# Performance work log

Hardware: AMD Instinct MI355X
Metric: run time of the kernel (lower is better)

The kernel has to match this reference:

```python
import jax, jax.numpy as jnp
import numpy as np

B, N, D_IN, D_OUT, H = 2, 2048, 1024, 1024, 16
HEAD_DIM = D_OUT // H


def setup_inputs() -> dict:
    key = jax.random.key(0)
    ks = jax.random.split(key, 8)
    s = 0.02
    return {
        "x": jax.random.normal(ks[0], (B, N, D_IN), dtype=jnp.float32),
        "Wq": jax.random.normal(ks[1], (D_IN, D_OUT), dtype=jnp.float32) * s,
        "Wk": jax.random.normal(ks[2], (D_IN, D_OUT), dtype=jnp.float32) * s,
        "Wv": jax.random.normal(ks[3], (D_IN, D_OUT), dtype=jnp.float32) * s,
        "Wo": jax.random.normal(ks[4], (D_OUT, D_OUT), dtype=jnp.float32) * s,
        "bo": jnp.zeros((D_OUT,), dtype=jnp.float32),
        "w": jax.random.uniform(ks[5], (H,), dtype=jnp.float32),
        "v": jax.random.uniform(ks[6], (H,), dtype=jnp.float32),
    }


def reference(x, Wq, Wk, Wv, Wo, bo, w, v):
    b, n, _ = x.shape
    h = w.shape[0]
    hd = Wq.shape[1] // h

    # QKV projections -> [b, h, n, hd]
    def proj(W):
        return (x @ W).reshape(b, n, h, hd).transpose(0, 2, 1, 3)

    q, k, val = proj(Wq), proj(Wk), proj(Wv)

    # relative-distance decay R_hat: [h, n, n]
    pos = jnp.arange(n)
    R = jnp.abs(pos[:, None] - pos[None, :]).astype(x.dtype)  # [n, n]
    wv = w[:, None, None]
    vv = v[:, None, None]
    R_hat = (1.0 + jnp.exp(vv)) / (1.0 + jnp.exp(vv - wv * R))  # [h, n, n]

    # ReLU(QK^T) * R_hat, causal mask, scaled softmax
    scores = jax.nn.relu(jnp.einsum("bhqd,bhkd->bhqk", q, k)) * R_hat[None]
    causal = jnp.triu(jnp.ones((n, n), dtype=bool), k=1)
    scores = jnp.where(causal[None, None], -jnp.inf, scores)
    attn = jax.nn.softmax(scores / np.sqrt(hd).astype(x.dtype), axis=-1)

    ctx = jnp.einsum("bhqk,bhkd->bhqd", attn, val)
    ctx = ctx.transpose(0, 2, 1, 3).reshape(b, n, h * hd)
    return ctx @ Wo + bo
```

## Files before the change

kernel.cpp:

```cpp
#include <hip/hip_runtime.h>

typedef unsigned short u16;
typedef unsigned int u32;
typedef __attribute__((ext_vector_type(8))) short bf16x8;
typedef __attribute__((ext_vector_type(4))) float f32x4;

__device__ __forceinline__ u16 f2bf(float f) {
    u32 u = __float_as_uint(f);
    u += 0x7fffu + ((u >> 16) & 1u);
    return (u16)(u >> 16);
}

#define GL2LDS(gp, lp)                                                                 \
    __builtin_amdgcn_global_load_lds((const __attribute__((address_space(1))) u32*)(const void*)(gp), \
                                     (__attribute__((address_space(3))) u32*)(void*)(lp), 16, 0, 0)

__global__ __launch_bounds__(256) void cast_kernel(const float* __restrict__ src,
                                                   u16* __restrict__ dst, int n4) {
    int i = blockIdx.x * 256 + threadIdx.x;
    if (i >= n4) return;
    float4 val = ((const float4*)src)[i];
    uint2 o;
    o.x = ((u32)f2bf(val.y) << 16) | f2bf(val.x);
    o.y = ((u32)f2bf(val.w) << 16) | f2bf(val.z);
    ((uint2*)dst)[i] = o;
}

__global__ __launch_bounds__(256) void transpose4(const float* __restrict__ Wq,
                                                  const float* __restrict__ Wk,
                                                  const float* __restrict__ Wv,
                                                  const float* __restrict__ Wo,
                                                  u16* __restrict__ Wcat,
                                                  u16* __restrict__ Wot) {
    __shared__ float tl[32][33];
    const int zi = blockIdx.z;
    const float* src = (zi == 0) ? Wq : (zi == 1) ? Wk : (zi == 2) ? Wv : Wo;
    u16* dst = (zi < 3) ? (Wcat + zi * 1048576) : Wot;
    const int tx = threadIdx.x & 31, ty = threadIdx.x >> 5;
    const int kt = blockIdx.y * 32, nt = blockIdx.x * 32;
#pragma unroll
    for (int j = 0; j < 4; ++j)
        tl[ty + j * 8][tx] = src[(kt + ty + j * 8) * 1024 + nt + tx];
    __syncthreads();
#pragma unroll
    for (int j = 0; j < 4; ++j)
        dst[(nt + ty + j * 8) * 1024 + kt + tx] = f2bf(tl[tx][ty + j * 8]);
}

__global__ __launch_bounds__(256) void transpose_v(const u16* __restrict__ src,
                                                   u16* __restrict__ dst) {
    __shared__ u16 tl[64][68];
    const int t = threadIdx.x, tx = t & 15, ty = t >> 4;
    const int rt = blockIdx.y * 64, ct = blockIdx.x * 64;
#pragma unroll
    for (int j = 0; j < 4; ++j) {
        const int row = ty + j * 16;
        uint2 vv = *(const uint2*)(src + (size_t)(rt + row) * 1024 + ct + tx * 4);
        tl[row][tx * 4 + 0] = (u16)(vv.x & 0xffff);
        tl[row][tx * 4 + 1] = (u16)(vv.x >> 16);
        tl[row][tx * 4 + 2] = (u16)(vv.y & 0xffff);
        tl[row][tx * 4 + 3] = (u16)(vv.y >> 16);
    }
    __syncthreads();
#pragma unroll
    for (int j = 0; j < 4; ++j) {
        const int c = ty + j * 16;
        uint2 o;
        o.x = (u32)tl[tx * 4 + 0][c] | ((u32)tl[tx * 4 + 1][c] << 16);
        o.y = (u32)tl[tx * 4 + 2][c] | ((u32)tl[tx * 4 + 3][c] << 16);
        *(uint2*)(dst + (size_t)(ct + c) * 4096 + rt + tx * 4) = o;
    }
}

__global__ __launch_bounds__(256) void rtab_kernel(const float* __restrict__ wp,
                                                   const float* __restrict__ vp,
                                                   float* __restrict__ tab,
                                                   u32* __restrict__ counter) {
    const int i = blockIdx.x * 256 + threadIdx.x;
    if (i == 0) counter[0] = 0u;
    const int h = i >> 11, d = i & 2047;
    const float vv = vp[h], ww = wp[h];
    tab[i] = (1.f + expf(vv)) / (1.f + expf(vv - ww * (float)d)) * 0.125f;
}

template <int MODE, int BN>
__global__ __launch_bounds__(256, 3) void gemm128(const u16* __restrict__ A,
                                                  const u16* __restrict__ Bt,
                                                  float* __restrict__ C,
                                                  const float* __restrict__ bias,
                                                  u16* __restrict__ Cb,
                                                  u16* __restrict__ Vrow,
                                                  int M, int N, int K) {
    constexpr int NBW = BN / 32;
    __shared__ __align__(16) u16 As[8192];
    __shared__ __align__(16) u16 Bs[BN * 64];
    const int t = threadIdx.x, lane = t & 63, wv = t >> 6;
    const int l15 = lane & 15, quad = lane >> 4;
    const int m0 = blockIdx.y << 7, n0 = blockIdx.x * BN;
    const int wm = (wv & 1) << 6, wn = (wv >> 1) * (BN / 2);

    f32x4 acc[4][NBW];
#pragma unroll
    for (int i = 0; i < 4; ++i)
#pragma unroll
        for (int j = 0; j < NBW; ++j) acc[i][j] = (f32x4){0.f, 0.f, 0.f, 0.f};

    const int lrow = lane >> 3, lchunk = lane & 7;
    for (int k0 = 0; k0 < K; k0 += 64) {
#pragma unroll
        for (int c = 0; c < 4; ++c) {
            const int r0 = wv * 32 + c * 8;
            const int row = r0 + lrow;
            const int g = lchunk ^ (row & 7);
            GL2LDS(A + (size_t)(m0 + row) * K + k0 + g * 8, &As[r0 * 64]);
        }
#pragma unroll
        for (int c = 0; c < BN / 32; ++c) {
            const int r0 = wv * (BN / 4) + c * 8;
            const int row = r0 + lrow;
            const int g = lchunk ^ (row & 7);
            GL2LDS(Bt + (size_t)(n0 + row) * K + k0 + g * 8, &Bs[r0 * 64]);
        }
        __syncthreads();
#pragma unroll
        for (int ks = 0; ks < 2; ++ks) {
            const int p = ((ks << 2) | quad) ^ (l15 & 7);
            bf16x8 af[4], bfr[NBW];
#pragma unroll
            for (int i = 0; i < 4; ++i)
                af[i] = *(const bf16x8*)&As[(wm + i * 16 + l15) * 64 + p * 8];
#pragma unroll
            for (int j = 0; j < NBW; ++j)
                bfr[j] = *(const bf16x8*)&Bs[(wn + j * 16 + l15) * 64 + p * 8];
#pragma unroll
            for (int mb = 0; mb < 4; ++mb)
#pragma unroll
                for (int nb = 0; nb < NBW; ++nb)
                    acc[mb][nb] = __builtin_amdgcn_mfma_f32_16x16x32_bf16(af[mb], bfr[nb],
                                                                          acc[mb][nb], 0, 0, 0);
        }
        __syncthreads();
    }
    const int rb = m0 + wm + (quad << 2);
    const int cbase = n0 + wn + l15;
#pragma unroll
    for (int mb = 0; mb < 4; ++mb)
#pragma unroll
        for (int nb = 0; nb < NBW; ++nb) {
            const int col = cbase + nb * 16;
#pragma unroll
            for (int r = 0; r < 4; ++r) {
                const int row = rb + mb * 16 + r;
                if (MODE == 0) {
                    C[(size_t)row * N + col] = acc[mb][nb][r] + bias[col];
                } else {
                    if (col < 2048)
                        Cb[(size_t)row * 2048 + col] = f2bf(acc[mb][nb][r]);
                    else
                        Vrow[(size_t)row * 1024 + (col - 2048)] = f2bf(acc[mb][nb][r]);
                }
            }
        }
}

__global__ __launch_bounds__(256, 3) void attn_kernel(const u16* __restrict__ qkb,
                                                      const u16* __restrict__ vtb,
                                                      const float* __restrict__ rtab,
                                                      u16* __restrict__ ctxb,
                                                      u32* __restrict__ counter) {
    __shared__ __align__(16) u16 Kt[2][4096];
    __shared__ __align__(16) u16 Vt2[2][4096];
    __shared__ float rall[2048];
    __shared__ int jobS;

    const int t = threadIdx.x, lane = t & 63, wv = t >> 6;
    const int l15 = lane & 15, quad = lane >> 4;
    const int lrow = lane >> 3, lchunk = lane & 7;
    const int half0 = (wv & 1) * 32;

    for (;;) {
        if (t == 0) jobS = (int)atomicAdd(counter, 1u);
        __syncthreads();
        const int job = jobS;
        if (job >= 1024) break;
        const int qt = 31 - (job >> 5);
        const int bh = job & 31;
        const int b = bh >> 4, h = bh & 15;
        const int q0 = qt << 6;

        for (int i = t; i < q0 + 64; i += 256) rall[i] = rtab[(h << 11) + i];

        bf16x8 qb[2];
        {
            const u16* qrow = qkb + (size_t)(b * 2048 + q0 + (wv << 4) + l15) * 2048 +
                              (h << 6) + quad * 8;
            qb[0] = *(const bf16x8*)(qrow);
            qb[1] = *(const bf16x8*)(qrow + 32);
        }

        f32x4 cacc[4];
#pragma unroll
        for (int i = 0; i < 4; ++i) cacc[i] = (f32x4){0.f, 0.f, 0.f, 0.f};
        float lacc = 0.f;

#pragma unroll
        for (int c = 0; c < 4; ++c) {
            const int r0 = half0 + c * 8;
            const int row = r0 + lrow;
            const int g = lchunk ^ (row & 7);
            if (wv < 2)
                GL2LDS(qkb + (size_t)(b * 2048 + row) * 2048 + 1024 + (h << 6) + g * 8,
                       &Kt[0][r0 * 64]);
            else
                GL2LDS(vtb + (size_t)((h << 6) + row) * 4096 + b * 2048 + g * 8,
                       &Vt2[0][r0 * 64]);
        }

        for (int kt = 0; kt <= qt; ++kt) {
            const int bsel = kt & 1;
            __syncthreads();
            if (kt < qt) {
                const int kg0 = (kt + 1) << 6;
#pragma unroll
                for (int c = 0; c < 4; ++c) {
                    const int r0 = half0 + c * 8;
                    const int row = r0 + lrow;
                    const int g = lchunk ^ (row & 7);
                    if (wv < 2)
                        GL2LDS(qkb + (size_t)(b * 2048 + kg0 + row) * 2048 + 1024 + (h << 6) + g * 8,
                               &Kt[bsel ^ 1][r0 * 64]);
                    else
                        GL2LDS(vtb + (size_t)((h << 6) + row) * 4096 + b * 2048 + kg0 + g * 8,
                               &Vt2[bsel ^ 1][r0 * 64]);
                }
            }

            f32x4 sacc[4];
#pragma unroll
            for (int i = 0; i < 4; ++i) sacc[i] = (f32x4){0.f, 0.f, 0.f, 0.f};
#pragma unroll
            for (int ks = 0; ks < 2; ++ks) {
                const int p = ((ks << 2) | quad) ^ (l15 & 7);
#pragma unroll
                for (int mb = 0; mb < 4; ++mb) {
                    bf16x8 ka = *(const bf16x8*)&Kt[bsel][(mb * 16 + l15) * 64 + p * 8];
                    sacc[mb] = __builtin_amdgcn_mfma_f32_16x16x32_bf16(ka, qb[ks],
                                                                       sacc[mb], 0, 0, 0);
                }
            }

            const int D0 = q0 - (kt << 6) + (wv << 4) + l15;
            u32 pk[4][2];
            if (kt < qt) {
#pragma unroll
                for (int mb = 0; mb < 4; ++mb) {
                    float pe[4];
#pragma unroll
                    for (int r = 0; r < 4; ++r) {
                        const int dist = D0 - (mb * 16 + (quad << 2) + r);
                        pe[r] = __expf(fmaxf(sacc[mb][r], 0.f) * rall[dist]);
                        lacc += pe[r];
                    }
                    pk[mb][0] = (__float_as_uint(pe[0]) >> 16) |
                                (__float_as_uint(pe[1]) & 0xffff0000u);
                    pk[mb][1] = (__float_as_uint(pe[2]) >> 16) |
                                (__float_as_uint(pe[3]) & 0xffff0000u);
                }
            } else {
#pragma unroll
                for (int mb = 0; mb < 4; ++mb) {
                    float pe[4];
#pragma unroll
                    for (int r = 0; r < 4; ++r) {
                        const int dist = D0 - (mb * 16 + (quad << 2) + r);
                        const int di = dist < 0 ? 0 : dist;
                        float p0 = __expf(fmaxf(sacc[mb][r], 0.f) * rall[di]);
                        pe[r] = (dist < 0) ? 0.f : p0;
                        lacc += pe[r];
                    }
                    pk[mb][0] = (__float_as_uint(pe[0]) >> 16) |
                                (__float_as_uint(pe[1]) & 0xffff0000u);
                    pk[mb][1] = (__float_as_uint(pe[2]) >> 16) |
                                (__float_as_uint(pe[3]) & 0xffff0000u);
                }
            }

#pragma unroll
            for (int ks = 0; ks < 2; ++ks) {
                int4 pv = {(int)pk[2 * ks][0], (int)pk[2 * ks][1],
                           (int)pk[2 * ks + 1][0], (int)pk[2 * ks + 1][1]};
                bf16x8 pb = *(bf16x8*)&pv;
                const int gA = (4 * ks + (quad >> 1)) ^ (l15 & 7);
                const int gB = (4 * ks + 2 + (quad >> 1)) ^ (l15 & 7);
                const int off = (quad & 1) * 4;
#pragma unroll
                for (int db = 0; db < 4; ++db) {
                    const u16* base = &Vt2[bsel][(db * 16 + l15) * 64];
                    uint2 va = *(const uint2*)(base + gA * 8 + off);
                    uint2 vb = *(const uint2*)(base + gB * 8 + off);
                    int4 vv = {(int)va.x, (int)va.y, (int)vb.x, (int)vb.y};
                    bf16x8 vf = *(bf16x8*)&vv;
                    cacc[db] = __builtin_amdgcn_mfma_f32_16x16x32_bf16(vf, pb,
                                                                       cacc[db], 0, 0, 0);
                }
            }
        }

        float lt = lacc;
        lt += __shfl_xor(lt, 16, 64);
        lt += __shfl_xor(lt, 32, 64);
        const float inv = 1.f / lt;
        u16* op = ctxb + (size_t)(b * 2048 + q0 + (wv << 4) + l15) * 1024 +
                  (h << 6) + (quad << 2);
#pragma unroll
        for (int db = 0; db < 4; ++db) {
            uint2 o;
            o.x = (u32)f2bf(cacc[db][0] * inv) | ((u32)f2bf(cacc[db][1] * inv) << 16);
            o.y = (u32)f2bf(cacc[db][2] * inv) | ((u32)f2bf(cacc[db][3] * inv) << 16);
            *(uint2*)(op + db * 16) = o;
        }
    }
}

extern "C" void kernel_launch(void* const* d_in, const int* in_sizes, int n_in,
                              void* d_out, int out_size, void* d_ws, size_t ws_size,
                              hipStream_t stream) {
    const float* x  = (const float*)d_in[0];
    const float* Wq = (const float*)d_in[1];
    const float* Wk = (const float*)d_in[2];
    const float* Wv = (const float*)d_in[3];
    const float* Wo = (const float*)d_in[4];
    const float* bo = (const float*)d_in[5];
    const float* w  = (const float*)d_in[6];
    const float* v  = (const float*)d_in[7];
    float* out = (float*)d_out;

    char* w8 = (char*)d_ws;
    u16*  xb   = (u16*)(w8);
    u16*  Wcat = (u16*)(w8 + (8u << 20));
    u16*  Wot  = (u16*)(w8 + (14u << 20));
    u16*  qkb  = (u16*)(w8 + (16u << 20));
    u16*  vtb  = (u16*)(w8 + (32u << 20));
    u16*  ctxb = (u16*)(w8 + (40u << 20));
    float* rtab = (float*)(w8 + (48u << 20));
    u32*  counter = (u32*)(w8 + (48u << 20) + (1u << 17));
    u16*  vrow = (u16*)(w8 + (49u << 20));

    cast_kernel<<<4096, 256, 0, stream>>>(x, xb, 1048576);
    transpose4<<<dim3(32, 32, 4), 256, 0, stream>>>(Wq, Wk, Wv, Wo, Wcat, Wot);
    rtab_kernel<<<128, 256, 0, stream>>>(w, v, rtab, counter);

    gemm128<1, 128><<<dim3(24, 32), 256, 0, stream>>>(xb, Wcat, nullptr, nullptr, qkb, vrow,
                                                      4096, 3072, 1024);
    transpose_v<<<dim3(16, 64), 256, 0, stream>>>(vrow, vtb);
    attn_kernel<<<768, 256, 0, stream>>>(qkb, vtb, rtab, ctxb, counter);
    gemm128<0, 64><<<dim3(16, 32), 256, 0, stream>>>(ctxb, Wot, out, bo, nullptr, nullptr,
                                                     4096, 1024, 1024);
}
```

Baseline: 193.3 us.

## Fuse V transpose into QKV GEMM epilogue, merge rtab into cast, single-buffer attention

The QKV GEMM now writes the V columns already transposed, staging the tile through swizzled LDS, so the separate transpose_v kernel and its round trip through memory go away. The rtab and counter init move into the cast kernel, removing another launch. The attention kernel drops K/V double buffering, which halves its LDS use, and raises occupancy to 6 blocks per CU with twice as many persistent blocks. The cost is that global loads no longer overlap the MFMA work and an extra barrier is added per tile.

```diff
diff --git a/kernel.cpp b/kernel.cpp
--- a/kernel.cpp
+++ b/kernel.cpp
@@ -16,8 +16,18 @@
                                      (__attribute__((address_space(3))) u32*)(void*)(lp), 16, 0, 0)
 
 __global__ __launch_bounds__(256) void cast_kernel(const float* __restrict__ src,
-                                                   u16* __restrict__ dst, int n4) {
+                                                   u16* __restrict__ dst, int n4,
+                                                   const float* __restrict__ wp,
+                                                   const float* __restrict__ vp,
+                                                   float* __restrict__ tab,
+                                                   u32* __restrict__ counter) {
     int i = blockIdx.x * 256 + threadIdx.x;
+    if (i == 0) counter[0] = 0u;
+    if (i < 32768) {
+        const int h = i >> 11, d = i & 2047;
+        const float vv = vp[h], ww = wp[h];
+        tab[i] = (1.f + expf(vv)) / (1.f + expf(vv - ww * (float)d)) * 0.125f;
+    }
     if (i >= n4) return;
     float4 val = ((const float4*)src)[i];
     uint2 o;
@@ -47,49 +57,13 @@
         dst[(nt + ty + j * 8) * 1024 + kt + tx] = f2bf(tl[tx][ty + j * 8]);
 }
 
-__global__ __launch_bounds__(256) void transpose_v(const u16* __restrict__ src,
-                                                   u16* __restrict__ dst) {
-    __shared__ u16 tl[64][68];
-    const int t = threadIdx.x, tx = t & 15, ty = t >> 4;
-    const int rt = blockIdx.y * 64, ct = blockIdx.x * 64;
-#pragma unroll
-    for (int j = 0; j < 4; ++j) {
-        const int row = ty + j * 16;
-        uint2 vv = *(const uint2*)(src + (size_t)(rt + row) * 1024 + ct + tx * 4);
-        tl[row][tx * 4 + 0] = (u16)(vv.x & 0xffff);
-        tl[row][tx * 4 + 1] = (u16)(vv.x >> 16);
-        tl[row][tx * 4 + 2] = (u16)(vv.y & 0xffff);
-        tl[row][tx * 4 + 3] = (u16)(vv.y >> 16);
-    }
-    __syncthreads();
-#pragma unroll
-    for (int j = 0; j < 4; ++j) {
-        const int c = ty + j * 16;
-        uint2 o;
-        o.x = (u32)tl[tx * 4 + 0][c] | ((u32)tl[tx * 4 + 1][c] << 16);
-        o.y = (u32)tl[tx * 4 + 2][c] | ((u32)tl[tx * 4 + 3][c] << 16);
-        *(uint2*)(dst + (size_t)(ct + c) * 4096 + rt + tx * 4) = o;
-    }
-}
-
-__global__ __launch_bounds__(256) void rtab_kernel(const float* __restrict__ wp,
-                                                   const float* __restrict__ vp,
-                                                   float* __restrict__ tab,
-                                                   u32* __restrict__ counter) {
-    const int i = blockIdx.x * 256 + threadIdx.x;
-    if (i == 0) counter[0] = 0u;
-    const int h = i >> 11, d = i & 2047;
-    const float vv = vp[h], ww = wp[h];
-    tab[i] = (1.f + expf(vv)) / (1.f + expf(vv - ww * (float)d)) * 0.125f;
-}
-
 template <int MODE, int BN>
 __global__ __launch_bounds__(256, 3) void gemm128(const u16* __restrict__ A,
                                                   const u16* __restrict__ Bt,
                                                   float* __restrict__ C,
                                                   const float* __restrict__ bias,
                                                   u16* __restrict__ Cb,
-                                                  u16* __restrict__ Vrow,
+                                                  u16* __restrict__ Vtb,
                                                   int M, int N, int K) {
     constexpr int NBW = BN / 32;
     __shared__ __align__(16) u16 As[8192];
@@ -141,6 +115,30 @@
         }
         __syncthreads();
     }
+    if (MODE == 1 && n0 >= 2048) {
+#pragma unroll
+        for (int mb = 0; mb < 4; ++mb)
+#pragma unroll
+            for (int nb = 0; nb < NBW; ++nb) {
+                const int c = wn + nb * 16 + l15;
+                u16* base = (c < 64 ? As : Bs) + (c & 63) * 128;
+#pragma unroll
+                for (int r = 0; r < 4; ++r) {
+                    const int rw = wm + mb * 16 + (quad << 2) + r;
+                    base[(((rw >> 3) ^ (c & 15)) << 3) + (rw & 7)] = f2bf(acc[mb][nb][r]);
+                }
+            }
+        __syncthreads();
+        const int c = t & 127, rseg = t >> 7;
+        const u16* base = (c < 64 ? As : Bs) + (c & 63) * 128;
+        u16* dst = Vtb + (size_t)(n0 - 2048 + c) * 4096 + m0 + rseg * 64;
+#pragma unroll
+        for (int ch = 0; ch < 8; ++ch) {
+            const int rc = rseg * 8 + ch;
+            *(uint4*)(dst + ch * 8) = *(const uint4*)&base[((rc ^ (c & 15)) << 3)];
+        }
+        return;
+    }
     const int rb = m0 + wm + (quad << 2);
     const int cbase = n0 + wn + l15;
 #pragma unroll
@@ -154,22 +152,19 @@
                 if (MODE == 0) {
                     C[(size_t)row * N + col] = acc[mb][nb][r] + bias[col];
                 } else {
-                    if (col < 2048)
-                        Cb[(size_t)row * 2048 + col] = f2bf(acc[mb][nb][r]);
-                    else
-                        Vrow[(size_t)row * 1024 + (col - 2048)] = f2bf(acc[mb][nb][r]);
-                }
-            }
-        }
-}
-
-__global__ __launch_bounds__(256, 3) void attn_kernel(const u16* __restrict__ qkb,
+                    Cb[(size_t)row * 2048 + col] = f2bf(acc[mb][nb][r]);
+                }
+            }
+        }
+}
+
+__global__ __launch_bounds__(256, 6) void attn_kernel(const u16* __restrict__ qkb,
                                                       const u16* __restrict__ vtb,
                                                       const float* __restrict__ rtab,
                                                       u16* __restrict__ ctxb,
                                                       u32* __restrict__ counter) {
-    __shared__ __align__(16) u16 Kt[2][4096];
-    __shared__ __align__(16) u16 Vt2[2][4096];
+    __shared__ __align__(16) u16 Kt[4096];
+    __shared__ __align__(16) u16 Vt[4096];
     __shared__ float rall[2048];
     __shared__ int jobS;
 
@@ -203,24 +198,10 @@
         for (int i = 0; i < 4; ++i) cacc[i] = (f32x4){0.f, 0.f, 0.f, 0.f};
         float lacc = 0.f;
 
-#pragma unroll
-        for (int c = 0; c < 4; ++c) {
-            const int r0 = half0 + c * 8;
-            const int row = r0 + lrow;
-            const int g = lchunk ^ (row & 7);
-            if (wv < 2)
-                GL2LDS(qkb + (size_t)(b * 2048 + row) * 2048 + 1024 + (h << 6) + g * 8,
-                       &Kt[0][r0 * 64]);
-            else
-                GL2LDS(vtb + (size_t)((h << 6) + row) * 4096 + b * 2048 + g * 8,
-                       &Vt2[0][r0 * 64]);
-        }
-
         for (int kt = 0; kt <= qt; ++kt) {
-            const int bsel = kt & 1;
+            const int kg0 = kt << 6;
             __syncthreads();
-            if (kt < qt) {
-                const int kg0 = (kt + 1) << 6;
+            {
 #pragma unroll
                 for (int c = 0; c < 4; ++c) {
                     const int r0 = half0 + c * 8;
@@ -228,12 +209,13 @@
                     const int g = lchunk ^ (row & 7);
                     if (wv < 2)
                         GL2LDS(qkb + (size_t)(b * 2048 + kg0 + row) * 2048 + 1024 + (h << 6) + g * 8,
-                               &Kt[bsel ^ 1][r0 * 64]);
+                               &Kt[r0 * 64]);
                     else
                         GL2LDS(vtb + (size_t)((h << 6) + row) * 4096 + b * 2048 + kg0 + g * 8,
-                               &Vt2[bsel ^ 1][r0 * 64]);
-                }
-            }
+                               &Vt[r0 * 64]);
+                }
+            }
+            __syncthreads();
 
             f32x4 sacc[4];
 #pragma unroll
@@ -243,13 +225,13 @@
                 const int p = ((ks << 2) | quad) ^ (l15 & 7);
 #pragma unroll
                 for (int mb = 0; mb < 4; ++mb) {
-                    bf16x8 ka = *(const bf16x8*)&Kt[bsel][(mb * 16 + l15) * 64 + p * 8];
+                    bf16x8 ka = *(const bf16x8*)&Kt[(mb * 16 + l15) * 64 + p * 8];
                     sacc[mb] = __builtin_amdgcn_mfma_f32_16x16x32_bf16(ka, qb[ks],
                                                                        sacc[mb], 0, 0, 0);
                 }
             }
 
-            const int D0 = q0 - (kt << 6) + (wv << 4) + l15;
+            const int D0 = q0 - kg0 + (wv << 4) + l15;
             u32 pk[4][2];
             if (kt < qt) {
 #pragma unroll
@@ -295,7 +277,7 @@
                 const int off = (quad & 1) * 4;
 #pragma unroll
                 for (int db = 0; db < 4; ++db) {
-                    const u16* base = &Vt2[bsel][(db * 16 + l15) * 64];
+                    const u16* base = &Vt[(db * 16 + l15) * 64];
                     uint2 va = *(const uint2*)(base + gA * 8 + off);
                     uint2 vb = *(const uint2*)(base + gB * 8 + off);
                     int4 vv = {(int)va.x, (int)va.y, (int)vb.x, (int)vb.y};
@@ -344,16 +326,13 @@
     u16*  ctxb = (u16*)(w8 + (40u << 20));
     float* rtab = (float*)(w8 + (48u << 20));
     u32*  counter = (u32*)(w8 + (48u << 20) + (1u << 17));
-    u16*  vrow = (u16*)(w8 + (49u << 20));
-
-    cast_kernel<<<4096, 256, 0, stream>>>(x, xb, 1048576);
+
+    cast_kernel<<<4096, 256, 0, stream>>>(x, xb, 1048576, w, v, rtab, counter);
     transpose4<<<dim3(32, 32, 4), 256, 0, stream>>>(Wq, Wk, Wv, Wo, Wcat, Wot);
-    rtab_kernel<<<128, 256, 0, stream>>>(w, v, rtab, counter);
-
-    gemm128<1, 128><<<dim3(24, 32), 256, 0, stream>>>(xb, Wcat, nullptr, nullptr, qkb, vrow,
+
+    gemm128<1, 128><<<dim3(24, 32), 256, 0, stream>>>(xb, Wcat, nullptr, nullptr, qkb, vtb,
                                                       4096, 3072, 1024);
-    transpose_v<<<dim3(16, 64), 256, 0, stream>>>(vrow, vtb);
-    attn_kernel<<<768, 256, 0, stream>>>(qkb, vtb, rtab, ctxb, counter);
+    attn_kernel<<<1536, 256, 0, stream>>>(qkb, vtb, rtab, ctxb, counter);
     gemm128<0, 64><<<dim3(16, 32), 256, 0, stream>>>(ctxb, Wot, out, bo, nullptr, nullptr,
                                                      4096, 1024, 1024);
 }
```

After: 224.5 us. +16.1%, slower.
